# Kernel optimization log

Hardware: AMD Instinct MI355X
Metric: run time of the kernel (lower is better)

Reference implementation:

```python
import jax, jax.numpy as jnp
import numpy as np

DIM = 512
N_HEADS = 8
HEAD_DIM = DIM // N_HEADS
BN_EPS = 1e-5


def setup_inputs() -> dict:
    key = jax.random.key(0)
    ks = jax.random.split(key, 8)
    B, C, H, W = 16, DIM, 32, 32
    x = jax.random.normal(ks[0], (B, C, H, W), dtype=jnp.float32)
    # 1x1 convs == channel matmuls: stacked q/k/v weights [3, out, in], proj [out, in]
    w_qkv = jax.random.normal(ks[1], (3, DIM, DIM), dtype=jnp.float32) * (DIM ** -0.5)
    w_proj = jax.random.normal(ks[2], (DIM, DIM), dtype=jnp.float32) * (DIM ** -0.5)
    # BatchNorm (inference form) params for q/k/v branches, stacked [3, C]
    bn_gamma = jax.random.uniform(ks[3], (3, DIM), minval=0.5, maxval=1.5)
    bn_beta = jax.random.normal(ks[4], (3, DIM)) * 0.1
    bn_mean = jax.random.normal(ks[5], (3, DIM)) * 0.1
    bn_var = jax.random.uniform(ks[6], (3, DIM), minval=0.5, maxval=1.5)
    return {"x": x, "w_qkv": w_qkv, "w_proj": w_proj, "bn_gamma": bn_gamma,
            "bn_beta": bn_beta, "bn_mean": bn_mean, "bn_var": bn_var}


def _ternary_ste(t):
    # forward: sign(t) in {-1,0,1}; backward: identity (straight-through)
    return t + jax.lax.stop_gradient(jnp.sign(t) - t)


def reference(x, w_qkv, w_proj, bn_gamma, bn_beta, bn_mean, bn_var):
    B, C, H, W = x.shape
    N = H * W
    xf = x.reshape(B, C, N)
    # fused 1x1 conv for q,k,v: [3,B,C,N]
    qkv = jnp.einsum('koc,bcn->kbon', w_qkv, xf)
    # BatchNorm (inference): y = (x - mean)/sqrt(var+eps)*gamma + beta
    s = bn_gamma / jnp.sqrt(bn_var + BN_EPS)          # [3,C]
    b = bn_beta - bn_mean * s                          # [3,C]
    qkv = qkv * s[:, None, :, None] + b[:, None, :, None]
    q = _ternary_ste(qkv[0]).reshape(B, N_HEADS, HEAD_DIM, N)
    k = _ternary_ste(qkv[1]).reshape(B, N_HEADS, HEAD_DIM, N)
    v = qkv[2].reshape(B, N_HEADS, HEAD_DIM, N)
    scale = HEAD_DIM ** -0.5
    attn = jnp.einsum('bhdn,bhen->bhde', q, k) * scale  # [B,h,d,d] channel-wise attn
    attn = jax.nn.softmax(attn, axis=-1)
    out = jnp.einsum('bhde,bhen->bhdn', attn, v).reshape(B, C, N)
    out = jnp.einsum('oc,bcn->bon', w_proj, out) + xf   # proj + residual
    return out.reshape(B, C, H, W)
```

## Files before the change

kernel.cpp:

```cpp
#include <hip/hip_runtime.h>
#include <math.h>

#define BN_EPS 1e-5f
#define FIXC 1.0e-4f

typedef _Float16 f16;
typedef _Float16 f16x4 __attribute__((ext_vector_type(4)));
typedef _Float16 f16x8 __attribute__((ext_vector_type(8)));
typedef float f32x4 __attribute__((ext_vector_type(4)));
typedef int i32x4 __attribute__((ext_vector_type(4)));

static constexpr int BB = 16;
static constexpr int C  = 512;
static constexpr int NP = 1024;
static constexpr int NH = 8;
static constexpr int HD = 64;
static constexpr int M3 = 1536;


static constexpr size_t OFF_WHI  = 0;
static constexpr size_t OFF_WLO  = 1572864;
static constexpr size_t OFF_WPH  = 3145728;
static constexpr size_t OFF_SB   = 3670016;
static constexpr size_t OFF_WN   = 3682304;
static constexpr size_t OFF_XN   = 3686400;
static constexpr size_t OFF_FLAG = 3751936;
static constexpr size_t OFF_XTH  = 5849088;
static constexpr size_t OFF_XTL  = 22626304;
static constexpr size_t OFF_AOT  = OFF_XTH;
static constexpr size_t OFF_Q    = 39403520;
static constexpr size_t OFF_K    = 47792128;
static constexpr size_t OFF_VT   = 56180736;

__device__ __forceinline__ void gld16(const void* g, void* l) {
  __builtin_amdgcn_global_load_lds(
      (const __attribute__((address_space(1))) void*)g,
      (__attribute__((address_space(3))) void*)l, 16, 0, 0);
}

__device__ __forceinline__ size_t frag_off(int tile, int kt, int row7, int k5) {
  return (((size_t)tile * 16 + kt) * 8 + (row7 >> 4)) * 512
       + (size_t)((row7 & 15) | ((k5 >> 3) << 4)) * 8;
}

__global__ __launch_bounds__(256) void k_convW(
    const float* __restrict__ wqkv, const float* __restrict__ wproj,
    const float* __restrict__ g, const float* __restrict__ be,
    const float* __restrict__ mu, const float* __restrict__ va,
    f16* __restrict__ Whi, f16* __restrict__ Wlo, f16* __restrict__ Wph,
    float* __restrict__ sA, float* __restrict__ bA, float* __restrict__ wnorm)
{
  const int i = blockIdx.x * 256 + threadIdx.x;
  {
    const int m = i >> 6, l = i & 63;
    const float4 v0 = *(const float4*)&wqkv[(size_t)m * C + l * 8];
    const float4 v1 = *(const float4*)&wqkv[(size_t)m * C + l * 8 + 4];
    const float vv[8] = {v0.x, v0.y, v0.z, v0.w, v1.x, v1.y, v1.z, v1.w};
    f16x8 hv, lv;
    float s2 = 0.f;
#pragma unroll
    for (int q = 0; q < 8; ++q) {
      const f16 h = (f16)vv[q];
      hv[q] = h; lv[q] = (f16)(vv[q] - (float)h);
      s2 = fmaf(vv[q], vv[q], s2);
    }
    *(f16x8*)&Whi[frag_off(m >> 7, l >> 2, m & 127, (l & 3) * 8)] = hv;
    *(f16x8*)&Wlo[(size_t)m * C + l * 8] = lv;
    if (m < 1024) {
      s2 += __shfl_xor(s2, 1);  s2 += __shfl_xor(s2, 2);
      s2 += __shfl_xor(s2, 4);  s2 += __shfl_xor(s2, 8);
      s2 += __shfl_xor(s2, 16); s2 += __shfl_xor(s2, 32);
      if (l == 0) wnorm[m] = sqrtf(s2);
    }
  }
  if (i < 32768) {
    const int m = i >> 6, l = i & 63;
    const float4 v0 = *(const float4*)&wproj[(size_t)m * C + l * 8];
    const float4 v1 = *(const float4*)&wproj[(size_t)m * C + l * 8 + 4];
    const float vv[8] = {v0.x, v0.y, v0.z, v0.w, v1.x, v1.y, v1.z, v1.w};
    f16x8 hv;
#pragma unroll
    for (int q = 0; q < 8; ++q) hv[q] = (f16)vv[q];
    *(f16x8*)&Wph[frag_off(m >> 7, l >> 2, m & 127, (l & 3) * 8)] = hv;
  }
  if (i < M3) {
    const float s = g[i] / sqrtf(va[i] + BN_EPS);
    sA[i] = s;
    bA[i] = be[i] - mu[i] * s;
  }
}

__global__ __launch_bounds__(256) void k_convX(
    const float* __restrict__ x, f16* __restrict__ XtH, f16* __restrict__ XtL,
    float* __restrict__ xnorm2)
{
  const int k0 = blockIdx.x * 64, n0 = blockIdx.y * 64, b = blockIdx.z;
  __shared__ float ls[64][65];
  const int t = threadIdx.x;
  const float* xp = x + ((size_t)b * C + k0) * NP + n0;
  const int c4 = (t & 15) * 4, r0 = t >> 4;
#pragma unroll
  for (int q = 0; q < 4; ++q) {
    const float4 v = *(const float4*)(xp + (size_t)(r0 + q * 16) * NP + c4);
    ls[r0 + q * 16][c4 + 0] = v.x; ls[r0 + q * 16][c4 + 1] = v.y;
    ls[r0 + q * 16][c4 + 2] = v.z; ls[r0 + q * 16][c4 + 3] = v.w;
  }
  __syncthreads();
  if (t < 64) {
    float s2 = 0.f;
#pragma unroll
    for (int q = 0; q < 64; ++q) { const float v = ls[q][t]; s2 = fmaf(v, v, s2); }
    atomicAdd(&xnorm2[(b << 10) + n0 + t], s2);
  }
  const int n = t >> 2, kk = (t & 3) * 16;
  const int n_abs = n0 + n;
  f16x8 hv0 = {}, hv1 = {}, lv0 = {}, lv1 = {};
#pragma unroll
  for (int q = 0; q < 8; ++q) {
    const float v = ls[kk + q][n];
    const f16 h = (f16)v;
    hv0[q] = h; lv0[q] = (f16)(v - (float)h);
  }
#pragma unroll
  for (int q = 0; q < 8; ++q) {
    const float v = ls[kk + 8 + q][n];
    const f16 h = (f16)v;
    hv1[q] = h; lv1[q] = (f16)(v - (float)h);
  }
  const int kb0 = k0 + kk, kb1 = k0 + kk + 8;
  *(f16x8*)&XtH[frag_off(b * 8 + (n_abs >> 7), kb0 >> 5, n_abs & 127, kb0 & 31)] = hv0;
  *(f16x8*)&XtH[frag_off(b * 8 + (n_abs >> 7), kb1 >> 5, n_abs & 127, kb1 & 31)] = hv1;
  *(f16x8*)&XtL[((size_t)b * NP + n_abs) * C + kb0] = lv0;
  *(f16x8*)&XtL[((size_t)b * NP + n_abs) * C + kb1] = lv1;
}

__global__ __launch_bounds__(256, 2) void k_qkv_mfma(
    const f16* __restrict__ Whi, const f16* __restrict__ XtH,
    const float* __restrict__ sA, const float* __restrict__ bA,
    const float* __restrict__ wnorm, const float* __restrict__ xnorm2,
    signed char* __restrict__ qw, signed char* __restrict__ kw,
    f16* __restrict__ vt, unsigned* __restrict__ flagbits)
{
  __shared__ __align__(16) f16 SMEM[8704];

  const int t = threadIdx.x, lane = t & 63, wid = t >> 6;
  const int n0 = blockIdx.x * 128, m0 = blockIdx.y * 128, b = blockIdx.z;

  const f16* Af = Whi + (size_t)(m0 >> 7) * 65536;
  const f16* Bf = XtH + ((size_t)b * 8 + (n0 >> 7)) * 65536;

  f32x4 acc[4][4];
#pragma unroll
  for (int i = 0; i < 4; ++i)
#pragma unroll
    for (int j = 0; j < 4; ++j) acc[i][j] = (f32x4){0.f, 0.f, 0.f, 0.f};

  const int wm = wid >> 1, wn = wid & 1;
  const int lr = lane & 15, ls = lane >> 4;

#define LOADF(KT, AR, BR) do {                                          \
    _Pragma("unroll")                                                   \
    for (int i_ = 0; i_ < 4; ++i_) {                                    \
      (AR)[i_] = *(const f16x8*)&Af[(size_t)(KT) * 4096 + (wm * 4 + i_) * 512 + lane * 8]; \
      (BR)[i_] = *(const f16x8*)&Bf[(size_t)(KT) * 4096 + (wn * 4 + i_) * 512 + lane * 8]; \
    }                                                                   \
  } while (0)

#define COMPF(AR, BR) do {                                              \
    _Pragma("unroll")                                                   \
    for (int i_ = 0; i_ < 4; ++i_)                                      \
      _Pragma("unroll")                                                 \
      for (int j_ = 0; j_ < 4; ++j_)                                    \
        acc[i_][j_] = __builtin_amdgcn_mfma_f32_16x16x32_f16(           \
            (AR)[i_], (BR)[j_], acc[i_][j_], 0, 0, 0);                  \
  } while (0)

  {
    f16x8 a0[4], b0[4], a1[4], b1[4], a2[4], b2[4];
    LOADF(0, a0, b0); LOADF(1, a1, b1);
    LOADF(2,  a2, b2); COMPF(a0, b0);
    LOADF(3,  a0, b0); COMPF(a1, b1);
    LOADF(4,  a1, b1); COMPF(a2, b2);
    LOADF(5,  a2, b2); COMPF(a0, b0);
    LOADF(6,  a0, b0); COMPF(a1, b1);
    LOADF(7,  a1, b1); COMPF(a2, b2);
    LOADF(8,  a2, b2); COMPF(a0, b0);
    LOADF(9,  a0, b0); COMPF(a1, b1);
    LOADF(10, a1, b1); COMPF(a2, b2);
    LOADF(11, a2, b2); COMPF(a0, b0);
    LOADF(12, a0, b0); COMPF(a1, b1);
    LOADF(13, a1, b1); COMPF(a2, b2);
    LOADF(14, a2, b2); COMPF(a0, b0);
    LOADF(15, a0, b0); COMPF(a1, b1);
    COMPF(a2, b2);
    COMPF(a0, b0);
  }

#undef LOADF
#undef COMPF

  const int kidx = m0 >> 9;
  if (kidx != 2) {
    signed char* dst0 = (kidx == 0) ? qw : kw;
    float xnrm[4];
#pragma unroll
    for (int j = 0; j < 4; ++j)
      xnrm[j] = sqrtf(xnorm2[(b << 10) + n0 + wn * 64 + j * 16 + lr]);
#pragma unroll
    for (int i = 0; i < 4; ++i) {
      float sv[4], bv[4], dl[4];
#pragma unroll
      for (int r = 0; r < 4; ++r) {
        const int o = m0 + wm * 64 + i * 16 + ls * 4 + r;
        sv[r] = sA[o]; bv[r] = bA[o];
        dl[r] = FIXC * wnorm[o] * sv[r];
      }
      const int oc0 = (m0 & 511) + wm * 64 + i * 16 + ls * 4;
      const int og0 = m0 + wm * 64 + i * 16 + ls * 4;
#pragma unroll
      for (int j = 0; j < 4; ++j) {
        const int n = n0 + wn * 64 + j * 16 + lr;
#pragma unroll
        for (int r = 0; r < 4; ++r) {
          const float z = fmaf(acc[i][j][r], sv[r], bv[r]);
          dst0[((size_t)b * C + oc0 + r) * NP + n] =
              (signed char)((z > 0.f) - (z < 0.f));
          if (fabsf(z) <= dl[r] * xnrm[j]) {
            const int of = og0 + r;
            atomicOr(&flagbits[(((size_t)b * NP + n) << 5) + (of >> 5)],
                     1u << (of & 31));
          }
        }
      }
    }
  } else {
    const int c0 = m0 & 511;
    for (int hf = 0; hf < 2; ++hf) {
      __syncthreads();
      if (wn == hf) {
#pragma unroll
        for (int i = 0; i < 4; ++i) {
          float sv[4], bv[4];
#pragma unroll
          for (int r = 0; r < 4; ++r) {
            const int o = m0 + wm * 64 + i * 16 + ls * 4 + r;
            sv[r] = sA[o]; bv[r] = bA[o];
          }
#pragma unroll
          for (int j = 0; j < 4; ++j) {
            f16x4 pk;
#pragma unroll
            for (int r = 0; r < 4; ++r)
              pk[r] = (f16)fmaf(acc[i][j][r], sv[r], bv[r]);
            *(f16x4*)&SMEM[(size_t)(j * 16 + lr) * 136 + wm * 64 + i * 16 + ls * 4] = pk;
          }
        }
      }
      __syncthreads();
      const int nl = t >> 2, cc = (t & 3) * 32;
      const f16* src = &SMEM[(size_t)nl * 136 + cc];
      f16x8 r0 = *(const f16x8*)(src + 0);
      f16x8 r1 = *(const f16x8*)(src + 8);
      f16x8 r2 = *(const f16x8*)(src + 16);
      f16x8 r3 = *(const f16x8*)(src + 24);
      f16* dstv = vt + ((size_t)b * NP + n0 + hf * 64 + nl) * C + c0 + cc;
      *(f16x8*)(dstv + 0)  = r0;
      *(f16x8*)(dstv + 8)  = r1;
      *(f16x8*)(dstv + 16) = r2;
      *(f16x8*)(dstv + 24) = r3;
    }
  }
}

__global__ __launch_bounds__(256) void k_fix(
    const unsigned* __restrict__ flagbits,
    const f16* __restrict__ Whi, const f16* __restrict__ Wlo,
    const f16* __restrict__ XtH, const f16* __restrict__ XtL,
    const float* __restrict__ sA, const float* __restrict__ bA,
    signed char* __restrict__ qw, signed char* __restrict__ kw)
{
  const int wv = blockIdx.x * 4 + (threadIdx.x >> 6);
  const int lane = threadIdx.x & 63;
  const int b = wv >> 10, n = wv & 1023;

  const unsigned* bm = flagbits + ((size_t)wv << 5);
  const unsigned myw = (lane < 32) ? bm[lane] : 0u;
  if (__ballot(myw != 0) == 0ULL) return;

  const int kb = lane * 8;
  const f16x8 bhv = *(const f16x8*)&XtH[
      frag_off(b * 8 + (n >> 7), kb >> 5, n & 127, kb & 31)];
  const f16x8 blv = *(const f16x8*)&XtL[((size_t)b * NP + n) * C + kb];
  float xv[8];
#pragma unroll
  for (int q = 0; q < 8; ++q) xv[q] = (float)bhv[q] + (float)blv[q];

  for (int w = 0; w < 32; ++w) {
    unsigned bits = __shfl(myw, w);
    while (bits) {
      const int o = w * 32 + __builtin_ctz(bits);
      bits &= bits - 1;
      const f16x8 ahv = *(const f16x8*)&Whi[
          frag_off(o >> 7, kb >> 5, o & 127, kb & 31)];
      const f16x8 alv = *(const f16x8*)&Wlo[(size_t)o * C + kb];
      float s = 0.f;
#pragma unroll
      for (int q = 0; q < 8; ++q)
        s = fmaf((float)ahv[q] + (float)alv[q], xv[q], s);
      s += __shfl_xor(s, 1);  s += __shfl_xor(s, 2);  s += __shfl_xor(s, 4);
      s += __shfl_xor(s, 8);  s += __shfl_xor(s, 16); s += __shfl_xor(s, 32);
      if (lane == 0) {
        const float y = fmaf(s, sA[o], bA[o]);
        const signed char sg = (signed char)((y > 0.f) - (y < 0.f));
        if (o < 512) qw[((size_t)b * C + o) * NP + n] = sg;
        else         kw[((size_t)b * C + (o - 512)) * NP + n] = sg;
      }
    }
  }
}

__global__ __launch_bounds__(256) void k_attn_fused(
    const signed char* __restrict__ qw, const signed char* __restrict__ kw,
    const f16* __restrict__ vt, f16* __restrict__ aot)
{
  const int quarter = blockIdx.x;
  const int bh = blockIdx.y;
  const int b = bh >> 3, h = bh & 7;
  const int t = threadIdx.x, lane = t & 63, wid = t >> 6;
  const int dw = wid * 16;
  const int lr = lane & 15, lg = lane >> 4;

  __shared__ f16 ph[64][72];
  __shared__ f16 pl[64][72];
  __shared__ f16 sb[64][72];

  const signed char* qp = qw + ((size_t)b * C + h * HD + dw + lr) * NP;
  const signed char* kp = kw + ((size_t)b * C + h * HD + lr) * NP;

  i32x4 accS[4];
#pragma unroll
  for (int j = 0; j < 4; ++j) accS[j] = (i32x4){0, 0, 0, 0};

#pragma unroll 4
  for (int ks = 0; ks < 16; ++ks) {
    const i32x4 af = *(const i32x4*)(qp + ks * 64 + lg * 16);
#pragma unroll
    for (int j = 0; j < 4; ++j) {
      const i32x4 bf = *(const i32x4*)(kp + (size_t)(j * 16) * NP + ks * 64 + lg * 16);
      accS[j] = __builtin_amdgcn_mfma_i32_16x16x64_i8(af, bf, accS[j], 0, 0, 0);
    }
  }

#pragma unroll
  for (int r = 0; r < 4; ++r) {
    float mx = (float)accS[0][r];
#pragma unroll
    for (int j = 1; j < 4; ++j) mx = fmaxf(mx, (float)accS[j][r]);
    mx = fmaxf(mx, __shfl_xor(mx, 1));
    mx = fmaxf(mx, __shfl_xor(mx, 2));
    mx = fmaxf(mx, __shfl_xor(mx, 4));
    mx = fmaxf(mx, __shfl_xor(mx, 8));
    float pvv[4];
    float sm = 0.f;
#pragma unroll
    for (int j = 0; j < 4; ++j) {
      pvv[j] = expf(((float)accS[j][r] - mx) * 0.125f);
      sm += pvv[j];
    }
    sm += __shfl_xor(sm, 1);
    sm += __shfl_xor(sm, 2);
    sm += __shfl_xor(sm, 4);
    sm += __shfl_xor(sm, 8);
    const float inv = 1.f / sm;
    const int drow = dw + lg * 4 + r;
#pragma unroll
    for (int j = 0; j < 4; ++j) {
      const float p = pvv[j] * inv;
      const f16 hi = (f16)p;
      ph[drow][j * 16 + lr] = hi;
      pl[drow][j * 16 + lr] = (f16)(p - (float)hi);
    }
  }
  __syncthreads();

  const f16x8 pa0h = *(const f16x8*)&ph[dw + lr][lg * 8];
  const f16x8 pa0l = *(const f16x8*)&pl[dw + lr][lg * 8];
  const f16x8 pa1h = *(const f16x8*)&ph[dw + lr][32 + lg * 8];
  const f16x8 pa1l = *(const f16x8*)&pl[dw + lr][32 + lg * 8];

  const f16* vbase = vt + (size_t)b * NP * C + h * HD;
  const int nbase = quarter * 256;

  for (int nc = 0; nc < 4; ++nc) {
    const int nn0 = nbase + nc * 64;
    __syncthreads();
#pragma unroll
    for (int nt = 0; nt < 4; ++nt) {
      const f16* vp = vbase + (size_t)(nn0 + nt * 16 + lr) * C + lg * 8;
      const f16x8 bv0 = *(const f16x8*)(vp);
      const f16x8 bv1 = *(const f16x8*)(vp + 32);
      f32x4 acc = (f32x4){0.f, 0.f, 0.f, 0.f};
      acc = __builtin_amdgcn_mfma_f32_16x16x32_f16(pa0h, bv0, acc, 0, 0, 0);
      acc = __builtin_amdgcn_mfma_f32_16x16x32_f16(pa0l, bv0, acc, 0, 0, 0);
      acc = __builtin_amdgcn_mfma_f32_16x16x32_f16(pa1h, bv1, acc, 0, 0, 0);
      acc = __builtin_amdgcn_mfma_f32_16x16x32_f16(pa1l, bv1, acc, 0, 0, 0);
      f16x4 pk;
#pragma unroll
      for (int r = 0; r < 4; ++r) pk[r] = (f16)acc[r];
      *(f16x4*)&sb[nt * 16 + lr][dw + lg * 4] = pk;
    }
    __syncthreads();
    const int nl = t >> 2, cc = (t & 3) * 16;
    const f16x8 o0 = *(const f16x8*)&sb[nl][cc];
    const f16x8 o1 = *(const f16x8*)&sb[nl][cc + 8];
    const int n_abs = nn0 + nl;
    const int c1 = h * HD + cc, c2 = h * HD + cc + 8;
    *(f16x8*)&aot[frag_off(b * 8 + (n_abs >> 7), c1 >> 5, n_abs & 127, c1 & 31)] = o0;
    *(f16x8*)&aot[frag_off(b * 8 + (n_abs >> 7), c2 >> 5, n_abs & 127, c2 & 31)] = o1;
  }
}

__global__ __launch_bounds__(256) void k_proj_mfma(
    const f16* __restrict__ Wph, const f16* __restrict__ aot,
    const float* __restrict__ X, float* __restrict__ out)
{
  __shared__ __align__(16) f16 SMEM[32768];
  f16* const As0 = SMEM;
  f16* const Bs0 = SMEM + 8192;
  f16* const As1 = SMEM + 16384;
  f16* const Bs1 = SMEM + 24576;

  const int t = threadIdx.x, lane = t & 63, wid = t >> 6;
  const int n0 = blockIdx.x * 128, m0 = blockIdx.y * 128, b = blockIdx.z;

  const f16* Af = Wph + (size_t)(m0 >> 7) * 65536;
  const f16* Bf = aot + ((size_t)b * 8 + (n0 >> 7)) * 65536;

  f32x4 acc[4][4];
#pragma unroll
  for (int i = 0; i < 4; ++i)
#pragma unroll
    for (int j = 0; j < 4; ++j) acc[i][j] = (f32x4){0.f, 0.f, 0.f, 0.f};

  const int wm = wid >> 1, wn = wid & 1;
  const int lr = lane & 15, ls = lane >> 4;
  const int soff = wid * 512 + lane * 8;

#define PSTAGE(TI, AS, BS) do {                                         \
    const f16* Ak_ = Af + (size_t)(TI) * 8192;                          \
    const f16* Bk_ = Bf + (size_t)(TI) * 8192;                          \
    _Pragma("unroll")                                                   \
    for (int r_ = 0; r_ < 4; ++r_) {                                    \
      gld16(Ak_ + r_ * 2048 + soff, &(AS)[r_ * 2048 + wid * 512]);      \
      gld16(Bk_ + r_ * 2048 + soff, &(BS)[r_ * 2048 + wid * 512]);      \
    }                                                                   \
  } while (0)

#define PCOMP(AS, BS) do {                                              \
    _Pragma("unroll")                                                   \
    for (int ksub_ = 0; ksub_ < 2; ++ksub_) {                           \
      f16x8 ah_[4], bh_[4];                                             \
      _Pragma("unroll")                                                 \
      for (int i_ = 0; i_ < 4; ++i_) {                                  \
        ah_[i_] = *(const f16x8*)&(AS)[ksub_ * 4096 + (wm * 4 + i_) * 512 + lane * 8]; \
        bh_[i_] = *(const f16x8*)&(BS)[ksub_ * 4096 + (wn * 4 + i_) * 512 + lane * 8]; \
      }                                                                 \
      _Pragma("unroll")                                                 \
      for (int i_ = 0; i_ < 4; ++i_)                                    \
        _Pragma("unroll")                                               \
        for (int j_ = 0; j_ < 4; ++j_)                                  \
          acc[i_][j_] = __builtin_amdgcn_mfma_f32_16x16x32_f16(         \
              ah_[i_], bh_[j_], acc[i_][j_], 0, 0, 0);                  \
    }                                                                   \
  } while (0)

  PSTAGE(0, As0, Bs0);
#pragma unroll
  for (int ti = 0; ti < 8; ++ti) {
    if (ti < 7) {
      if (ti & 1) PSTAGE(ti + 1, As0, Bs0);
      else        PSTAGE(ti + 1, As1, Bs1);
      asm volatile("s_waitcnt vmcnt(8)" ::: "memory");
    } else {
      asm volatile("s_waitcnt vmcnt(0)" ::: "memory");
    }
    __builtin_amdgcn_sched_barrier(0);
    __builtin_amdgcn_s_barrier();
    if (ti & 1) PCOMP(As1, Bs1); else PCOMP(As0, Bs0);
    asm volatile("s_waitcnt lgkmcnt(0)" ::: "memory");
    __builtin_amdgcn_sched_barrier(0);
    __builtin_amdgcn_s_barrier();
  }

#undef PSTAGE
#undef PCOMP

#pragma unroll
  for (int i = 0; i < 4; ++i) {
    const int oc0 = m0 + wm * 64 + i * 16 + ls * 4;
#pragma unroll
    for (int j = 0; j < 4; ++j) {
      const int n = n0 + wn * 64 + j * 16 + lr;
#pragma unroll
      for (int r = 0; r < 4; ++r) {
        const size_t idx = ((size_t)b * C + oc0 + r) * NP + n;
        out[idx] = acc[i][j][r] + X[idx];
      }
    }
  }
}

extern "C" void kernel_launch(void* const* d_in, const int* in_sizes, int n_in,
                              void* d_out, int out_size, void* d_ws, size_t ws_size,
                              hipStream_t stream)
{
  const float* x      = (const float*)d_in[0];
  const float* w_qkv  = (const float*)d_in[1];
  const float* w_proj = (const float*)d_in[2];
  const float* g      = (const float*)d_in[3];
  const float* be     = (const float*)d_in[4];
  const float* mu     = (const float*)d_in[5];
  const float* va     = (const float*)d_in[6];
  float* out = (float*)d_out;

  char* ws = (char*)d_ws;
  f16*  Whi = (f16*)(ws + OFF_WHI);
  f16*  Wlo = (f16*)(ws + OFF_WLO);
  f16*  Wph = (f16*)(ws + OFF_WPH);
  float* sA = (float*)(ws + OFF_SB);
  float* bA = sA + M3;
  float* wn = (float*)(ws + OFF_WN);
  float* xn2 = (float*)(ws + OFF_XN);
  unsigned* flagbits = (unsigned*)(ws + OFF_FLAG);
  f16*  XtH = (f16*)(ws + OFF_XTH);
  f16*  XtL = (f16*)(ws + OFF_XTL);
  f16*  aot = (f16*)(ws + OFF_AOT);
  signed char* qw = (signed char*)(ws + OFF_Q);
  signed char* kw = (signed char*)(ws + OFF_K);
  f16*  vtw = (f16*)(ws + OFF_VT);

  hipMemsetAsync(xn2, 0, OFF_XTH - OFF_XN, stream);

  k_convW<<<dim3(384), 256, 0, stream>>>(
      w_qkv, w_proj, g, be, mu, va, Whi, Wlo, Wph, sA, bA, wn);
  k_convX<<<dim3(C / 64, NP / 64, BB), 256, 0, stream>>>(x, XtH, XtL, xn2);
  k_qkv_mfma<<<dim3(NP / 128, M3 / 128, BB), 256, 0, stream>>>(
      Whi, XtH, sA, bA, wn, xn2, qw, kw, vtw, flagbits);
  k_fix<<<dim3(BB * NP / 4), 256, 0, stream>>>(
      flagbits, Whi, Wlo, XtH, XtL, sA, bA, qw, kw);
  k_attn_fused<<<dim3(4, BB * NH), 256, 0, stream>>>(qw, kw, vtw, aot);
  k_proj_mfma<<<dim3(NP / 128, C / 128, BB), 256, 0, stream>>>(Wph, aot, x, out);
}
```

Before: 142.6 us.

## Halve QKV GEMM M-tile for occupancy and give attention blocks larger N ranges

The QKV MFMA kernel now uses 64x128 output tiles instead of 128x128, with fewer accumulators, a double-buffered register pipeline in place of the triple-buffered one, and a higher launch-bounds occupancy hint. The V-transpose epilogue is simplified to a single shared-memory pass. The attention kernel is launched with 2 N-halves instead of 4 quarters, so each block recomputes the q·k softmax half as often. In exchange, the GEMM re-reads X tiles twice as often, and the attention kernel has fewer blocks to spread across the GPU.

New measurement: 146.1 us. +2.5%, slower.

```diff
diff --git a/kernel.cpp b/kernel.cpp
--- a/kernel.cpp
+++ b/kernel.cpp
@@ -134,41 +134,44 @@
   *(f16x8*)&XtL[((size_t)b * NP + n_abs) * C + kb1] = lv1;
 }
 
-__global__ __launch_bounds__(256, 2) void k_qkv_mfma(
+__global__ __launch_bounds__(256, 4) void k_qkv_mfma(
     const f16* __restrict__ Whi, const f16* __restrict__ XtH,
     const float* __restrict__ sA, const float* __restrict__ bA,
     const float* __restrict__ wnorm, const float* __restrict__ xnorm2,
     signed char* __restrict__ qw, signed char* __restrict__ kw,
     f16* __restrict__ vt, unsigned* __restrict__ flagbits)
 {
-  __shared__ __align__(16) f16 SMEM[8704];
+  __shared__ __align__(16) f16 SMEM[128 * 72];
 
   const int t = threadIdx.x, lane = t & 63, wid = t >> 6;
-  const int n0 = blockIdx.x * 128, m0 = blockIdx.y * 128, b = blockIdx.z;
+  const int n0 = blockIdx.x * 128, m0 = blockIdx.y * 64, b = blockIdx.z;
 
   const f16* Af = Whi + (size_t)(m0 >> 7) * 65536;
   const f16* Bf = XtH + ((size_t)b * 8 + (n0 >> 7)) * 65536;
 
-  f32x4 acc[4][4];
-#pragma unroll
-  for (int i = 0; i < 4; ++i)
+  f32x4 acc[2][4];
+#pragma unroll
+  for (int i = 0; i < 2; ++i)
 #pragma unroll
     for (int j = 0; j < 4; ++j) acc[i][j] = (f32x4){0.f, 0.f, 0.f, 0.f};
 
   const int wm = wid >> 1, wn = wid & 1;
   const int lr = lane & 15, ls = lane >> 4;
+  const int ablk0 = ((m0 & 64) >> 4) + wm * 2;
+  const int bblk0 = wn * 4;
 
 #define LOADF(KT, AR, BR) do {                                          \
     _Pragma("unroll")                                                   \
-    for (int i_ = 0; i_ < 4; ++i_) {                                    \
-      (AR)[i_] = *(const f16x8*)&Af[(size_t)(KT) * 4096 + (wm * 4 + i_) * 512 + lane * 8]; \
-      (BR)[i_] = *(const f16x8*)&Bf[(size_t)(KT) * 4096 + (wn * 4 + i_) * 512 + lane * 8]; \
-    }                                                                   \
+    for (int i_ = 0; i_ < 2; ++i_)                                      \
+      (AR)[i_] = *(const f16x8*)&Af[((size_t)(KT) * 8 + ablk0 + i_) * 512 + lane * 8]; \
+    _Pragma("unroll")                                                   \
+    for (int j_ = 0; j_ < 4; ++j_)                                      \
+      (BR)[j_] = *(const f16x8*)&Bf[((size_t)(KT) * 8 + bblk0 + j_) * 512 + lane * 8]; \
   } while (0)
 
 #define COMPF(AR, BR) do {                                              \
     _Pragma("unroll")                                                   \
-    for (int i_ = 0; i_ < 4; ++i_)                                      \
+    for (int i_ = 0; i_ < 2; ++i_)                                      \
       _Pragma("unroll")                                                 \
       for (int j_ = 0; j_ < 4; ++j_)                                    \
         acc[i_][j_] = __builtin_amdgcn_mfma_f32_16x16x32_f16(           \
@@ -176,24 +179,15 @@
   } while (0)
 
   {
-    f16x8 a0[4], b0[4], a1[4], b1[4], a2[4], b2[4];
-    LOADF(0, a0, b0); LOADF(1, a1, b1);
-    LOADF(2,  a2, b2); COMPF(a0, b0);
-    LOADF(3,  a0, b0); COMPF(a1, b1);
-    LOADF(4,  a1, b1); COMPF(a2, b2);
-    LOADF(5,  a2, b2); COMPF(a0, b0);
-    LOADF(6,  a0, b0); COMPF(a1, b1);
-    LOADF(7,  a1, b1); COMPF(a2, b2);
-    LOADF(8,  a2, b2); COMPF(a0, b0);
-    LOADF(9,  a0, b0); COMPF(a1, b1);
-    LOADF(10, a1, b1); COMPF(a2, b2);
-    LOADF(11, a2, b2); COMPF(a0, b0);
-    LOADF(12, a0, b0); COMPF(a1, b1);
-    LOADF(13, a1, b1); COMPF(a2, b2);
-    LOADF(14, a2, b2); COMPF(a0, b0);
-    LOADF(15, a0, b0); COMPF(a1, b1);
-    COMPF(a2, b2);
-    COMPF(a0, b0);
+    f16x8 a0[2], b0[4], a1[2], b1[4];
+    LOADF(0, a0, b0);
+#pragma unroll
+    for (int kt = 0; kt < 16; kt += 2) {
+      LOADF(kt + 1, a1, b1);
+      COMPF(a0, b0);
+      if (kt + 2 < 16) LOADF(kt + 2, a0, b0);
+      COMPF(a1, b1);
+    }
   }
 
 #undef LOADF
@@ -207,16 +201,16 @@
     for (int j = 0; j < 4; ++j)
       xnrm[j] = sqrtf(xnorm2[(b << 10) + n0 + wn * 64 + j * 16 + lr]);
 #pragma unroll
-    for (int i = 0; i < 4; ++i) {
+    for (int i = 0; i < 2; ++i) {
       float sv[4], bv[4], dl[4];
 #pragma unroll
       for (int r = 0; r < 4; ++r) {
-        const int o = m0 + wm * 64 + i * 16 + ls * 4 + r;
+        const int o = m0 + wm * 32 + i * 16 + ls * 4 + r;
         sv[r] = sA[o]; bv[r] = bA[o];
         dl[r] = FIXC * wnorm[o] * sv[r];
       }
-      const int oc0 = (m0 & 511) + wm * 64 + i * 16 + ls * 4;
-      const int og0 = m0 + wm * 64 + i * 16 + ls * 4;
+      const int oc0 = (m0 & 511) + wm * 32 + i * 16 + ls * 4;
+      const int og0 = m0 + wm * 32 + i * 16 + ls * 4;
 #pragma unroll
       for (int j = 0; j < 4; ++j) {
         const int n = n0 + wn * 64 + j * 16 + lr;
@@ -235,40 +229,37 @@
     }
   } else {
     const int c0 = m0 & 511;
-    for (int hf = 0; hf < 2; ++hf) {
-      __syncthreads();
-      if (wn == hf) {
-#pragma unroll
-        for (int i = 0; i < 4; ++i) {
-          float sv[4], bv[4];
-#pragma unroll
-          for (int r = 0; r < 4; ++r) {
-            const int o = m0 + wm * 64 + i * 16 + ls * 4 + r;
-            sv[r] = sA[o]; bv[r] = bA[o];
-          }
-#pragma unroll
-          for (int j = 0; j < 4; ++j) {
-            f16x4 pk;
-#pragma unroll
-            for (int r = 0; r < 4; ++r)
-              pk[r] = (f16)fmaf(acc[i][j][r], sv[r], bv[r]);
-            *(f16x4*)&SMEM[(size_t)(j * 16 + lr) * 136 + wm * 64 + i * 16 + ls * 4] = pk;
-          }
-        }
+#pragma unroll
+    for (int i = 0; i < 2; ++i) {
+      float sv[4], bv[4];
+#pragma unroll
+      for (int r = 0; r < 4; ++r) {
+        const int o = m0 + wm * 32 + i * 16 + ls * 4 + r;
+        sv[r] = sA[o]; bv[r] = bA[o];
       }
-      __syncthreads();
-      const int nl = t >> 2, cc = (t & 3) * 32;
-      const f16* src = &SMEM[(size_t)nl * 136 + cc];
-      f16x8 r0 = *(const f16x8*)(src + 0);
-      f16x8 r1 = *(const f16x8*)(src + 8);
-      f16x8 r2 = *(const f16x8*)(src + 16);
-      f16x8 r3 = *(const f16x8*)(src + 24);
-      f16* dstv = vt + ((size_t)b * NP + n0 + hf * 64 + nl) * C + c0 + cc;
-      *(f16x8*)(dstv + 0)  = r0;
-      *(f16x8*)(dstv + 8)  = r1;
-      *(f16x8*)(dstv + 16) = r2;
-      *(f16x8*)(dstv + 24) = r3;
-    }
+      const int clocal = wm * 32 + i * 16 + ls * 4;
+#pragma unroll
+      for (int j = 0; j < 4; ++j) {
+        const int nlocal = wn * 64 + j * 16 + lr;
+        f16x4 pk;
+#pragma unroll
+        for (int r = 0; r < 4; ++r)
+          pk[r] = (f16)fmaf(acc[i][j][r], sv[r], bv[r]);
+        *(f16x4*)&SMEM[(size_t)nlocal * 72 + clocal] = pk;
+      }
+    }
+    __syncthreads();
+    const int nl = t >> 1, cc = (t & 1) * 32;
+    const f16* src = &SMEM[(size_t)nl * 72 + cc];
+    f16x8 r0 = *(const f16x8*)(src + 0);
+    f16x8 r1 = *(const f16x8*)(src + 8);
+    f16x8 r2 = *(const f16x8*)(src + 16);
+    f16x8 r3 = *(const f16x8*)(src + 24);
+    f16* dstv = vt + ((size_t)b * NP + n0 + nl) * C + c0 + cc;
+    *(f16x8*)(dstv + 0)  = r0;
+    *(f16x8*)(dstv + 8)  = r1;
+    *(f16x8*)(dstv + 16) = r2;
+    *(f16x8*)(dstv + 24) = r3;
   }
 }
 
@@ -323,7 +314,7 @@
     const signed char* __restrict__ qw, const signed char* __restrict__ kw,
     const f16* __restrict__ vt, f16* __restrict__ aot)
 {
-  const int quarter = blockIdx.x;
+  const int half = blockIdx.x;
   const int bh = blockIdx.y;
   const int b = bh >> 3, h = bh & 7;
   const int t = threadIdx.x, lane = t & 63, wid = t >> 6;
@@ -389,9 +380,9 @@
   const f16x8 pa1l = *(const f16x8*)&pl[dw + lr][32 + lg * 8];
 
   const f16* vbase = vt + (size_t)b * NP * C + h * HD;
-  const int nbase = quarter * 256;
-
-  for (int nc = 0; nc < 4; ++nc) {
+  const int nbase = half * 512;
+
+  for (int nc = 0; nc < 8; ++nc) {
     const int nn0 = nbase + nc * 64;
     __syncthreads();
 #pragma unroll
@@ -544,10 +535,10 @@
   k_convW<<<dim3(384), 256, 0, stream>>>(
       w_qkv, w_proj, g, be, mu, va, Whi, Wlo, Wph, sA, bA, wn);
   k_convX<<<dim3(C / 64, NP / 64, BB), 256, 0, stream>>>(x, XtH, XtL, xn2);
-  k_qkv_mfma<<<dim3(NP / 128, M3 / 128, BB), 256, 0, stream>>>(
+  k_qkv_mfma<<<dim3(NP / 128, M3 / 64, BB), 256, 0, stream>>>(
       Whi, XtH, sA, bA, wn, xn2, qw, kw, vtw, flagbits);
   k_fix<<<dim3(BB * NP / 4), 256, 0, stream>>>(
       flagbits, Whi, Wlo, XtH, XtL, sA, bA, qw, kw);
-  k_attn_fused<<<dim3(4, BB * NH), 256, 0, stream>>>(qw, kw, vtw, aot);
+  k_attn_fused<<<dim3(2, BB * NH), 256, 0, stream>>>(qw, kw, vtw, aot);
   k_proj_mfma<<<dim3(NP / 128, C / 128, BB), 256, 0, stream>>>(Wph, aot, x, out);
 }
```

## Swizzle block IDs across XCDs and halve attention grid split

Applied to the files above, without the earlier changes.

Flattens the qkv and projection GEMM grids to 1D and remaps block IDs so consecutive blocks on the same XCD share weight and activation tiles, aiming at better L2 reuse on the chiplet layout. The attention kernel now splits each batch-head into halves instead of quarters, so the per-block score and softmax work is repeated less often, at the cost of fewer blocks in flight. The qkv GEMM main loop is also rewritten from a three-buffer unrolled register pipeline into a two-buffer loop, which lowers register pressure but hides less load latency.

After: 139.2 us. 2.4% less time.

```diff
diff --git a/kernel.cpp b/kernel.cpp
--- a/kernel.cpp
+++ b/kernel.cpp
@@ -43,6 +43,10 @@
        + (size_t)((row7 & 15) | ((k5 >> 3) << 4)) * 8;
 }
 
+__device__ __forceinline__ int xcd_swz(int id, int chunk) {
+  return (id & 7) * chunk + (id >> 3);
+}
+
 __global__ __launch_bounds__(256) void k_convW(
     const float* __restrict__ wqkv, const float* __restrict__ wproj,
     const float* __restrict__ g, const float* __restrict__ be,
@@ -143,11 +147,16 @@
 {
   __shared__ __align__(16) f16 SMEM[8704];
 
+  const int swz = xcd_swz(blockIdx.x, 192);
+  const int mi = swz % 12;
+  const int ni = (swz / 12) & 7;
+  const int b  = swz / 96;
+  const int n0 = ni * 128, m0 = mi * 128;
+
   const int t = threadIdx.x, lane = t & 63, wid = t >> 6;
-  const int n0 = blockIdx.x * 128, m0 = blockIdx.y * 128, b = blockIdx.z;
-
-  const f16* Af = Whi + (size_t)(m0 >> 7) * 65536;
-  const f16* Bf = XtH + ((size_t)b * 8 + (n0 >> 7)) * 65536;
+
+  const f16* Af = Whi + (size_t)mi * 65536;
+  const f16* Bf = XtH + ((size_t)b * 8 + ni) * 65536;
 
   f32x4 acc[4][4];
 #pragma unroll
@@ -161,8 +170,8 @@
 #define LOADF(KT, AR, BR) do {                                          \
     _Pragma("unroll")                                                   \
     for (int i_ = 0; i_ < 4; ++i_) {                                    \
-      (AR)[i_] = *(const f16x8*)&Af[(size_t)(KT) * 4096 + (wm * 4 + i_) * 512 + lane * 8]; \
-      (BR)[i_] = *(const f16x8*)&Bf[(size_t)(KT) * 4096 + (wn * 4 + i_) * 512 + lane * 8]; \
+      (AR)[i_] = *(const f16x8*)&Af[((size_t)(KT) * 8 + wm * 4 + i_) * 512 + lane * 8]; \
+      (BR)[i_] = *(const f16x8*)&Bf[((size_t)(KT) * 8 + wn * 4 + i_) * 512 + lane * 8]; \
     }                                                                   \
   } while (0)
 
@@ -176,24 +185,15 @@
   } while (0)
 
   {
-    f16x8 a0[4], b0[4], a1[4], b1[4], a2[4], b2[4];
-    LOADF(0, a0, b0); LOADF(1, a1, b1);
-    LOADF(2,  a2, b2); COMPF(a0, b0);
-    LOADF(3,  a0, b0); COMPF(a1, b1);
-    LOADF(4,  a1, b1); COMPF(a2, b2);
-    LOADF(5,  a2, b2); COMPF(a0, b0);
-    LOADF(6,  a0, b0); COMPF(a1, b1);
-    LOADF(7,  a1, b1); COMPF(a2, b2);
-    LOADF(8,  a2, b2); COMPF(a0, b0);
-    LOADF(9,  a0, b0); COMPF(a1, b1);
-    LOADF(10, a1, b1); COMPF(a2, b2);
-    LOADF(11, a2, b2); COMPF(a0, b0);
-    LOADF(12, a0, b0); COMPF(a1, b1);
-    LOADF(13, a1, b1); COMPF(a2, b2);
-    LOADF(14, a2, b2); COMPF(a0, b0);
-    LOADF(15, a0, b0); COMPF(a1, b1);
-    COMPF(a2, b2);
-    COMPF(a0, b0);
+    f16x8 a0[4], b0[4], a1[4], b1[4];
+    LOADF(0, a0, b0);
+#pragma unroll
+    for (int kt = 0; kt < 16; kt += 2) {
+      LOADF(kt + 1, a1, b1);
+      COMPF(a0, b0);
+      if (kt + 2 < 16) LOADF(kt + 2, a0, b0);
+      COMPF(a1, b1);
+    }
   }
 
 #undef LOADF
@@ -323,8 +323,9 @@
     const signed char* __restrict__ qw, const signed char* __restrict__ kw,
     const f16* __restrict__ vt, f16* __restrict__ aot)
 {
-  const int quarter = blockIdx.x;
-  const int bh = blockIdx.y;
+  const int swz = xcd_swz(blockIdx.x, 32);
+  const int half = swz & 1;
+  const int bh = swz >> 1;
   const int b = bh >> 3, h = bh & 7;
   const int t = threadIdx.x, lane = t & 63, wid = t >> 6;
   const int dw = wid * 16;
@@ -389,9 +390,9 @@
   const f16x8 pa1l = *(const f16x8*)&pl[dw + lr][32 + lg * 8];
 
   const f16* vbase = vt + (size_t)b * NP * C + h * HD;
-  const int nbase = quarter * 256;
-
-  for (int nc = 0; nc < 4; ++nc) {
+  const int nbase = half * 512;
+
+  for (int nc = 0; nc < 8; ++nc) {
     const int nn0 = nbase + nc * 64;
     __syncthreads();
 #pragma unroll
@@ -430,11 +431,16 @@
   f16* const As1 = SMEM + 16384;
   f16* const Bs1 = SMEM + 24576;
 
+  const int swz = xcd_swz(blockIdx.x, 64);
+  const int mi = swz & 3;
+  const int ni = (swz >> 2) & 7;
+  const int b  = swz >> 5;
+  const int n0 = ni * 128, m0 = mi * 128;
+
   const int t = threadIdx.x, lane = t & 63, wid = t >> 6;
-  const int n0 = blockIdx.x * 128, m0 = blockIdx.y * 128, b = blockIdx.z;
-
-  const f16* Af = Wph + (size_t)(m0 >> 7) * 65536;
-  const f16* Bf = aot + ((size_t)b * 8 + (n0 >> 7)) * 65536;
+
+  const f16* Af = Wph + (size_t)mi * 65536;
+  const f16* Bf = aot + ((size_t)b * 8 + ni) * 65536;
 
   f32x4 acc[4][4];
 #pragma unroll
@@ -544,10 +550,10 @@
   k_convW<<<dim3(384), 256, 0, stream>>>(
       w_qkv, w_proj, g, be, mu, va, Whi, Wlo, Wph, sA, bA, wn);
   k_convX<<<dim3(C / 64, NP / 64, BB), 256, 0, stream>>>(x, XtH, XtL, xn2);
-  k_qkv_mfma<<<dim3(NP / 128, M3 / 128, BB), 256, 0, stream>>>(
+  k_qkv_mfma<<<dim3(1536), 256, 0, stream>>>(
       Whi, XtH, sA, bA, wn, xn2, qw, kw, vtw, flagbits);
   k_fix<<<dim3(BB * NP / 4), 256, 0, stream>>>(
       flagbits, Whi, Wlo, XtH, XtL, sA, bA, qw, kw);
-  k_attn_fused<<<dim3(4, BB * NH), 256, 0, stream>>>(qw, kw, vtw, aot);
-  k_proj_mfma<<<dim3(NP / 128, C / 128, BB), 256, 0, stream>>>(Wph, aot, x, out);
-}
+  k_attn_fused<<<dim3(256), 256, 0, stream>>>(qw, kw, vtw, aot);
+  k_proj_mfma<<<dim3(512), 256, 0, stream>>>(Wph, aot, x, out);
+}
```
